# Kernel optimization log

Hardware: AMD Instinct MI355X
Metric: run time of the kernel (lower is better)

Reference implementation:

```python
import jax, jax.numpy as jnp
import numpy as np

B, T = 4096, 16384
KLEN = 50          # min(50, n_steps) with dt=1
REFRACTORY = 3.0   # self.refractory / self.dt


def setup_inputs() -> dict:
    key = jax.random.key(0)
    k1, = jax.random.split(key, 1)
    # scale so that v_reset + I_filtered/100 can cross v_th (=-55 vs reset -70)
    I_input = jax.random.normal(k1, (B, T), dtype=jnp.float32) * 2000.0
    return {
        "I_input": I_input,
        "tau_m": jnp.float32(10.0),
        "tau_s": jnp.float32(5.0),
        "v_th": jnp.float32(-55.0),
        "v_reset": jnp.float32(-70.0),
        "eta": jnp.float32(-5.0),
    }


def _srm_spikes(I_input, tau_m, tau_s, v_th, v_reset, eta):
    # synaptic kernel: (exp(-t/tau_m) - exp(-t/tau_s)) / sum
    t = jnp.arange(KLEN, dtype=jnp.float32)
    kernel = jnp.exp(-t / tau_m) - jnp.exp(-t / tau_s)
    kernel = kernel / (jnp.sum(kernel) + 1e-10)
    # 'same' convolution per trace (np.convolve semantics: kernel flipped)
    I_filt = jax.vmap(lambda x: jnp.convolve(x, kernel, mode="same"))(I_input)

    def step(ref, I_t):
        # ref: [B] refractory countdown; I_t: [B] filtered current at time t
        in_ref = ref > 0
        v_free = v_reset + I_t / 100.0
        spike = jnp.where(jnp.logical_and(~in_ref, v_free >= v_th), 1.0, 0.0)
        new_ref = jnp.where(in_ref, ref - 1.0,
                            jnp.where(spike > 0, REFRACTORY, 0.0))
        return new_ref, spike

    ref0 = jnp.zeros((I_input.shape[0],), dtype=jnp.float32)
    # original loop runs t = 1 .. n_steps-1; spikes[0] stays 0
    _, spikes_t = jax.lax.scan(step, ref0, jnp.swapaxes(I_filt[:, 1:], 0, 1))
    spikes = jnp.concatenate(
        [jnp.zeros((I_input.shape[0], 1), dtype=jnp.float32),
         jnp.swapaxes(spikes_t, 0, 1)], axis=1)
    return spikes


def reference(I_input, tau_m, tau_s, v_th, v_reset, eta):
    return _srm_spikes(I_input, tau_m, tau_s, v_th, v_reset, eta)
```

## Files before the change

### kernel.cpp

```cpp
#include <hip/hip_runtime.h>


#define TLEN   16384
#define NROWS  4096
#define KLEN   50
#define WPB    4
#define SEGS   16
#define SEGLEN 1024
#define TILEB  272

#define FGRP  256
#define FNGRP 64
#define TILEW 336

#define WS_FLAGS_OFF 256
#define WS_NEED (WS_FLAGS_OFF + (size_t)NROWS * SEGS * sizeof(int))

typedef float f4 __attribute__((ext_vector_type(4)));

__device__ __forceinline__ float uniformf(float x) {
    return __int_as_float(__builtin_amdgcn_readfirstlane(__float_as_int(x)));
}

__device__ __forceinline__ int swz(int b) { return b ^ ((b >> 4) & 7); }

__device__ __forceinline__ int map_compose(int first, int then) {
    int r = 0;
#pragma unroll
    for (int s = 0; s < 4; ++s) {
        int a = (first >> (2 * s)) & 3;
        int b = (then >> (2 * a)) & 3;
        r |= b << (2 * s);
    }
    return r;
}

__device__ float solve_thresh(float v_reset, float v_th) {
    auto tokey = [](float f) {
        unsigned u = __float_as_uint(f);
        return (u & 0x80000000u) ? ~u : (u | 0x80000000u);
    };
    auto fromkey = [](unsigned k) {
        unsigned u = (k & 0x80000000u) ? (k & 0x7FFFFFFFu) : ~k;
        return __uint_as_float(u);
    };
    const float maxf = 3.402823466e38f;
    unsigned lo = tokey(-maxf), hi = tokey(maxf);
    if (!((v_reset + maxf / 100.0f) >= v_th))
        return __uint_as_float(0x7F800000u);
    while (lo < hi) {
        unsigned mid = lo + ((hi - lo) >> 1);
        float a = fromkey(mid);
        if ((v_reset + a / 100.0f) >= v_th) hi = mid;
        else lo = mid + 1;
    }
    return fromkey(lo);
}

__global__ __launch_bounds__(64)
void setup_kernel(const float* __restrict__ p_tau_m,
                  const float* __restrict__ p_tau_s,
                  const float* __restrict__ p_v_th,
                  const float* __restrict__ p_v_reset,
                  float* __restrict__ wsf)
{
    const int lane = threadIdx.x & 63;
    const float tau_m = p_tau_m[0];
    const float tau_s = p_tau_s[0];

    float ft = (float)lane;
    float v = (lane < KLEN) ? (expf(-ft / tau_m) - expf(-ft / tau_s)) : 0.0f;

    float ksum = 0.0f;
    for (int t = 0; t < KLEN; ++t)
        ksum += __shfl(v, t, 64);
    const float kden = ksum + 1e-10f;
    const float kt = v / kden;

    if (lane < KLEN) wsf[lane] = kt;
    if (lane == 0)   wsf[KLEN] = solve_thresh(p_v_reset[0], p_v_th[0]);
}

__global__ __launch_bounds__(256)
void conv_kernel(const float* __restrict__ I,
                 const float* __restrict__ wsf,
                 float* __restrict__ out,
                 int* __restrict__ flags)
{
    __shared__ __align__(16) float tile[WPB][TILEB * 4];

    const int lane = threadIdx.x & 63;
    const int wid  = threadIdx.x >> 6;
    const int wg   = blockIdx.x * WPB + wid;
    const int row  = wg >> 4;
    const int seg  = wg & 15;

    float kt[KLEN];
#pragma unroll
    for (int t = 0; t < KLEN; ++t) kt[t] = wsf[t];
    const float athr = wsf[KLEN];

    const float* Irow = I + (size_t)row * TLEN;
    float* Orow = out + (size_t)row * TLEN;

    const int pos0 = seg * SEGLEN;
    const int t0   = pos0 + 16 * lane;

    char* tb_ = (char*)&tile[wid][0];

#pragma unroll
    for (int j = 0; j < 4; ++j) {
        f4 v = *(const f4*)(Irow + pos0 + 4 * lane + 256 * j);
        *(f4*)(tb_ + (swz(7 + lane + 64 * j) << 4)) = v;
    }
    if (lane < 7) {
        f4 h = (f4){0.0f, 0.0f, 0.0f, 0.0f};
        if (pos0 > 0) h = *(const f4*)(Irow + pos0 - 28 + 4 * lane);
        *(f4*)(tb_ + (swz(lane) << 4)) = h;
    }
    if (lane >= 57 && lane < 63) {
        f4 h = (f4){0.0f, 0.0f, 0.0f, 0.0f};
        if (pos0 + SEGLEN < TLEN)
            h = *(const f4*)(Irow + pos0 + SEGLEN + 4 * (lane - 57));
        *(f4*)(tb_ + (swz(lane + 206) << 4)) = h;
    }

    f4 wv[17];
#pragma unroll
    for (int i = 0; i < 17; ++i)
        wv[i] = *(const f4*)(tb_ + (swz(4 * lane + i) << 4));
#define WIN(m) (wv[(m) >> 2][(m) & 3])

    float acc[16];
#pragma unroll
    for (int k = 0; k < 16; ++k) acc[k] = 0.0f;
#pragma unroll
    for (int o = -25; o <= 39; ++o) {
        const float wx = WIN(o + 28);
#pragma unroll
        for (int k = 0; k < 16; ++k) {
            const int jj = k + 24 - o;
            if (jj >= 0 && jj < KLEN)
                acc[k] = fmaf(kt[jj], wx, acc[k]);
        }
    }
#undef WIN

    int m16 = 0;
#pragma unroll
    for (int k = 0; k < 16; ++k)
        m16 |= (acc[k] >= athr) ? (1 << k) : 0;
    if (t0 == 0) m16 &= ~1;
    const int rowflag = m16;

    const int sh = 4 * (lane & 3);
#pragma unroll
    for (int j = 0; j < 4; ++j) {
        const int bits = __shfl(m16, (lane >> 2) + 16 * j, 64);
        f4 o0;
        o0.x = ((bits >> (sh + 0)) & 1) ? 1.0f : 0.0f;
        o0.y = ((bits >> (sh + 1)) & 1) ? 1.0f : 0.0f;
        o0.z = ((bits >> (sh + 2)) & 1) ? 1.0f : 0.0f;
        o0.w = ((bits >> (sh + 3)) & 1) ? 1.0f : 0.0f;
        *(f4*)(Orow + pos0 + 4 * lane + 256 * j) = o0;
    }

    const unsigned long long anyb = __ballot(rowflag != 0);
    if (lane == 0) flags[wg] = (anyb != 0ULL) ? 1 : 0;
}

__global__ __launch_bounds__(256)
void fixup_kernel(const int* __restrict__ flags,
                  float* __restrict__ out)
{
    const int lane = threadIdx.x & 63;
    const int wid  = threadIdx.x >> 6;
    const int row  = blockIdx.x * WPB + wid;

    const int* pf = flags + SEGS * row;
    int any = 0;
#pragma unroll
    for (int j = 0; j < SEGS; ++j) any |= pf[j];
    if (any == 0) return;

    float* Orow = out + (size_t)row * TLEN;
    int r0 = 0;

    for (int g = 0; g < FNGRP; ++g) {
        f4 o = *(const f4*)(Orow + g * FGRP + 4 * lane);
        int cand[4];
        cand[0] = (o.x != 0.0f);
        cand[1] = (o.y != 0.0f);
        cand[2] = (o.z != 0.0f);
        cand[3] = (o.w != 0.0f);

        const int cm = cand[0] | cand[1] | cand[2] | cand[3];
        const unsigned long long anyc = __ballot(cm != 0);
        if (anyc == 0ULL) { r0 = 0; continue; }

        int s0 = 0, s1 = 1, s2 = 2, s3 = 3;
#pragma unroll
        for (int k = 0; k < 4; ++k) {
            const int c3 = cand[k] ? 3 : 0;
            s0 = (s0 > 0) ? (s0 - 1) : c3;
            s1 = (s1 > 0) ? (s1 - 1) : c3;
            s2 = (s2 > 0) ? (s2 - 1) : c3;
            s3 = (s3 > 0) ? (s3 - 1) : c3;
        }
        int P = s0 | (s1 << 2) | (s2 << 4) | (s3 << 6);

#pragma unroll
        for (int d = 1; d < 64; d <<= 1) {
            const int prev = __shfl_up(P, d, 64);
            const int comp = map_compose(prev, P);
            P = (lane >= d) ? comp : P;
        }
        const int Pprev = __shfl_up(P, 1, 64);
        const int sin0  = (lane == 0) ? r0 : ((Pprev >> (2 * r0)) & 3);
        const int Pfull = __shfl(P, 63, 64);
        r0 = (Pfull >> (2 * r0)) & 3;

        int s = sin0;
        float sp[4];
#pragma unroll
        for (int k = 0; k < 4; ++k) {
            const int spike = (s == 0) & cand[k];
            sp[k] = spike ? 1.0f : 0.0f;
            s = (s > 0) ? (s - 1) : (cand[k] ? 3 : 0);
        }
        f4 o0; o0.x = sp[0]; o0.y = sp[1]; o0.z = sp[2]; o0.w = sp[3];
        *(f4*)(Orow + g * FGRP + 4 * lane) = o0;
    }
}

__global__ __launch_bounds__(256)
void srm_kernel(const float* __restrict__ I,
                const float* __restrict__ p_tau_m,
                const float* __restrict__ p_tau_s,
                const float* __restrict__ p_v_th,
                const float* __restrict__ p_v_reset,
                float* __restrict__ out)
{
    __shared__ __align__(16) float tile[WPB][2][TILEW];

    const int lane = threadIdx.x & 63;
    const int wid  = threadIdx.x >> 6;
    const int row  = blockIdx.x * WPB + wid;

    const float tau_m   = p_tau_m[0];
    const float tau_s   = p_tau_s[0];
    const float v_th    = p_v_th[0];
    const float v_reset = p_v_reset[0];

    float ku[KLEN];
    float ksum = 0.0f;
#pragma unroll
    for (int t = 0; t < KLEN; ++t) {
        float ft = (float)t;
        float v = expf(-ft / tau_m) - expf(-ft / tau_s);
        ksum += v;
        ku[t] = uniformf(v);
    }
    const float kden = uniformf(ksum + 1e-10f);
    float kt[KLEN];
#pragma unroll
    for (int t = 0; t < KLEN; ++t) kt[t] = uniformf(ku[t] / kden);

    const float athr = uniformf(solve_thresh(v_reset, v_th));

    const float* Irow = I + (size_t)row * TLEN;
    float* Orow = out + (size_t)row * TLEN;

    float Cv[4], Nv[4], Lv[4];
    {
        f4 a = *(const f4*)(Irow + 0 * FGRP + 4 * lane);
        Cv[0] = a.x; Cv[1] = a.y; Cv[2] = a.z; Cv[3] = a.w;
        f4 c = *(const f4*)(Irow + 1 * FGRP + 4 * lane);
        Nv[0] = c.x; Nv[1] = c.y; Nv[2] = c.z; Nv[3] = c.w;
    }

    if (lane < 8) {
        f4 z = (f4){0.0f, 0.0f, 0.0f, 0.0f};
        *(f4*)&tile[wid][0][4 * lane] = z;
    }
    {
        f4 c; c.x = Cv[0]; c.y = Cv[1]; c.z = Cv[2]; c.w = Cv[3];
        *(f4*)&tile[wid][0][32 + 4 * lane] = c;
    }

    int r0 = 0;

    for (int g = 0; g < FNGRP; ++g) {
        const int cur = g & 1;
        const int nxt = cur ^ 1;

        if (g + 2 < FNGRP) {
            f4 a = *(const f4*)(Irow + (size_t)(g + 2) * FGRP + 4 * lane);
            Lv[0] = a.x; Lv[1] = a.y; Lv[2] = a.z; Lv[3] = a.w;
        } else {
            Lv[0] = Lv[1] = Lv[2] = Lv[3] = 0.0f;
        }

        f4 nv; nv.x = Nv[0]; nv.y = Nv[1]; nv.z = Nv[2]; nv.w = Nv[3];
        if (lane < 8)
            *(f4*)&tile[wid][cur][288 + 4 * lane] = nv;
        *(f4*)&tile[wid][nxt][32 + 4 * lane] = nv;
        if (lane >= 56) {
            f4 cv; cv.x = Cv[0]; cv.y = Cv[1]; cv.z = Cv[2]; cv.w = Cv[3];
            *(f4*)&tile[wid][nxt][4 * (lane - 56)] = cv;
        }

        f4 wv[15];
#pragma unroll
        for (int i = 0; i < 15; ++i)
            wv[i] = *(const f4*)&tile[wid][cur][4 * lane + 4 + 4 * i];
#define WIN(m) (wv[(m) >> 2][(m) & 3])

        float acc[4];
        acc[0] = acc[1] = acc[2] = acc[3] = 0.0f;
#pragma unroll
        for (int o = -25; o <= 27; ++o) {
            const float w = WIN(o + 28);
#pragma unroll
            for (int k = 0; k < 4; ++k) {
                const int jj = k + 24 - o;
                if (jj >= 0 && jj < KLEN)
                    acc[k] = fmaf(kt[jj], w, acc[k]);
            }
        }
#undef WIN

        const int tb = g * FGRP + 4 * lane;
        int cand[4];
#pragma unroll
        for (int k = 0; k < 4; ++k)
            cand[k] = (acc[k] >= athr) ? 1 : 0;
        cand[0] &= (tb != 0);

        const int cm = cand[0] | cand[1] | cand[2] | cand[3];
        const unsigned long long anyc = __ballot(cm != 0);

        f4 o0;
        if (anyc == 0ULL) {
            o0 = (f4){0.0f, 0.0f, 0.0f, 0.0f};
            r0 = 0;
        } else {
            int s0 = 0, s1 = 1, s2 = 2, s3 = 3;
#pragma unroll
            for (int k = 0; k < 4; ++k) {
                const int c3 = cand[k] ? 3 : 0;
                s0 = (s0 > 0) ? (s0 - 1) : c3;
                s1 = (s1 > 0) ? (s1 - 1) : c3;
                s2 = (s2 > 0) ? (s2 - 1) : c3;
                s3 = (s3 > 0) ? (s3 - 1) : c3;
            }
            int P = s0 | (s1 << 2) | (s2 << 4) | (s3 << 6);
#pragma unroll
            for (int d = 1; d < 64; d <<= 1) {
                const int prev = __shfl_up(P, d, 64);
                const int comp = map_compose(prev, P);
                P = (lane >= d) ? comp : P;
            }
            const int Pprev = __shfl_up(P, 1, 64);
            const int sin0  = (lane == 0) ? r0 : ((Pprev >> (2 * r0)) & 3);
            const int Pfull = __shfl(P, 63, 64);
            r0 = (Pfull >> (2 * r0)) & 3;

            int s = sin0;
            float sp[4];
#pragma unroll
            for (int k = 0; k < 4; ++k) {
                const int spike = (s == 0) & cand[k];
                sp[k] = spike ? 1.0f : 0.0f;
                s = (s > 0) ? (s - 1) : (cand[k] ? 3 : 0);
            }
            o0.x = sp[0]; o0.y = sp[1]; o0.z = sp[2]; o0.w = sp[3];
        }

        *(f4*)(Orow + tb) = o0;

#pragma unroll
        for (int j = 0; j < 4; ++j) { Cv[j] = Nv[j]; Nv[j] = Lv[j]; }
    }
}

extern "C" void kernel_launch(void* const* d_in, const int* in_sizes, int n_in,
                              void* d_out, int out_size, void* d_ws, size_t ws_size,
                              hipStream_t stream) {
    const float* I       = (const float*)d_in[0];
    const float* tau_m   = (const float*)d_in[1];
    const float* tau_s   = (const float*)d_in[2];
    const float* v_th    = (const float*)d_in[3];
    const float* v_reset = (const float*)d_in[4];
    float* out = (float*)d_out;

    if (ws_size >= WS_NEED) {
        float* wsf  = (float*)d_ws;
        int* flags  = (int*)((char*)d_ws + WS_FLAGS_OFF);
        setup_kernel<<<dim3(1), dim3(64), 0, stream>>>(
            tau_m, tau_s, v_th, v_reset, wsf);
        conv_kernel<<<dim3(NROWS * SEGS / WPB), dim3(256), 0, stream>>>(
            I, wsf, out, flags);
        fixup_kernel<<<dim3(NROWS / WPB), dim3(256), 0, stream>>>(flags, out);
    } else {
        srm_kernel<<<dim3(NROWS / WPB), dim3(256), 0, stream>>>(
            I, tau_m, tau_s, v_th, v_reset, out);
    }
}
```

Before: 150.7 us.

## Loop each wave over 8 segments with register prefetch of next segment

Each wavefront now processes eight consecutive 1024-sample segments of a row instead of one. The global loads for the next segment are issued into registers before the current segment's convolution runs, to hide memory latency. This also amortises the per-wave kernel-tap loads and cuts the flag count to two per row. In exchange the grid shrinks eightfold to 2048 blocks, which may reduce occupancy and latency hiding across waves, and register pressure rises from the prefetch buffers.

After: 214.7 us. +42.5%, slower.

```diff
diff --git a/kernel.cpp b/kernel.cpp
--- a/kernel.cpp
+++ b/kernel.cpp
@@ -5,7 +5,8 @@
 #define NROWS  4096
 #define KLEN   50
 #define WPB    4
-#define SEGS   16
+#define CHK    2
+#define SPW    8
 #define SEGLEN 1024
 #define TILEB  272
 
@@ -14,7 +15,7 @@
 #define TILEW 336
 
 #define WS_FLAGS_OFF 256
-#define WS_NEED (WS_FLAGS_OFF + (size_t)NROWS * SEGS * sizeof(int))
+#define WS_NEED (WS_FLAGS_OFF + (size_t)NROWS * CHK * sizeof(int))
 
 typedef float f4 __attribute__((ext_vector_type(4)));
 
@@ -92,8 +93,9 @@
     const int lane = threadIdx.x & 63;
     const int wid  = threadIdx.x >> 6;
     const int wg   = blockIdx.x * WPB + wid;
-    const int row  = wg >> 4;
-    const int seg  = wg & 15;
+    const int row  = wg >> 1;
+    const int half = wg & 1;
+    const int base = half * (SPW * SEGLEN);
 
     float kt[KLEN];
 #pragma unroll
@@ -103,66 +105,88 @@
     const float* Irow = I + (size_t)row * TLEN;
     float* Orow = out + (size_t)row * TLEN;
 
-    const int pos0 = seg * SEGLEN;
-    const int t0   = pos0 + 16 * lane;
-
     char* tb_ = (char*)&tile[wid][0];
 
-#pragma unroll
-    for (int j = 0; j < 4; ++j) {
-        f4 v = *(const f4*)(Irow + pos0 + 4 * lane + 256 * j);
-        *(f4*)(tb_ + (swz(7 + lane + 64 * j) << 4)) = v;
-    }
-    if (lane < 7) {
-        f4 h = (f4){0.0f, 0.0f, 0.0f, 0.0f};
-        if (pos0 > 0) h = *(const f4*)(Irow + pos0 - 28 + 4 * lane);
-        *(f4*)(tb_ + (swz(lane) << 4)) = h;
-    }
-    if (lane >= 57 && lane < 63) {
-        f4 h = (f4){0.0f, 0.0f, 0.0f, 0.0f};
-        if (pos0 + SEGLEN < TLEN)
-            h = *(const f4*)(Irow + pos0 + SEGLEN + 4 * (lane - 57));
-        *(f4*)(tb_ + (swz(lane + 206) << 4)) = h;
-    }
-
-    f4 wv[17];
-#pragma unroll
-    for (int i = 0; i < 17; ++i)
-        wv[i] = *(const f4*)(tb_ + (swz(4 * lane + i) << 4));
+    f4 pre[4], phl, phr;
+    {
+        const int p0 = base;
+#pragma unroll
+        for (int j = 0; j < 4; ++j)
+            pre[j] = *(const f4*)(Irow + p0 + 4 * lane + 256 * j);
+        phl = (f4){0.0f, 0.0f, 0.0f, 0.0f};
+        phr = (f4){0.0f, 0.0f, 0.0f, 0.0f};
+        if (lane < 7 && p0 > 0)
+            phl = *(const f4*)(Irow + p0 - 28 + 4 * lane);
+        if (lane >= 57 && lane < 63 && p0 + SEGLEN < TLEN)
+            phr = *(const f4*)(Irow + p0 + SEGLEN + 4 * (lane - 57));
+    }
+
+    int rowflag = 0;
+
+    for (int g = 0; g < SPW; ++g) {
+        const int pos0 = base + g * SEGLEN;
+        const int t0   = pos0 + 16 * lane;
+
+#pragma unroll
+        for (int j = 0; j < 4; ++j)
+            *(f4*)(tb_ + (swz(7 + lane + 64 * j) << 4)) = pre[j];
+        if (lane < 7)
+            *(f4*)(tb_ + (swz(lane) << 4)) = phl;
+        if (lane >= 57 && lane < 63)
+            *(f4*)(tb_ + (swz(lane + 206) << 4)) = phr;
+
+        if (g < SPW - 1) {
+            const int p1 = pos0 + SEGLEN;
+#pragma unroll
+            for (int j = 0; j < 4; ++j)
+                pre[j] = *(const f4*)(Irow + p1 + 4 * lane + 256 * j);
+            phl = (f4){0.0f, 0.0f, 0.0f, 0.0f};
+            phr = (f4){0.0f, 0.0f, 0.0f, 0.0f};
+            if (lane < 7)
+                phl = *(const f4*)(Irow + p1 - 28 + 4 * lane);
+            if (lane >= 57 && lane < 63 && p1 + SEGLEN < TLEN)
+                phr = *(const f4*)(Irow + p1 + SEGLEN + 4 * (lane - 57));
+        }
+
+        f4 wv[17];
+#pragma unroll
+        for (int i = 0; i < 17; ++i)
+            wv[i] = *(const f4*)(tb_ + (swz(4 * lane + i) << 4));
 #define WIN(m) (wv[(m) >> 2][(m) & 3])
 
-    float acc[16];
-#pragma unroll
-    for (int k = 0; k < 16; ++k) acc[k] = 0.0f;
-#pragma unroll
-    for (int o = -25; o <= 39; ++o) {
-        const float wx = WIN(o + 28);
-#pragma unroll
-        for (int k = 0; k < 16; ++k) {
-            const int jj = k + 24 - o;
-            if (jj >= 0 && jj < KLEN)
-                acc[k] = fmaf(kt[jj], wx, acc[k]);
-        }
-    }
+        float acc[16];
+#pragma unroll
+        for (int k = 0; k < 16; ++k) acc[k] = 0.0f;
+#pragma unroll
+        for (int o = -25; o <= 39; ++o) {
+            const float wx = WIN(o + 28);
+#pragma unroll
+            for (int k = 0; k < 16; ++k) {
+                const int jj = k + 24 - o;
+                if (jj >= 0 && jj < KLEN)
+                    acc[k] = fmaf(kt[jj], wx, acc[k]);
+            }
+        }
 #undef WIN
 
-    int m16 = 0;
-#pragma unroll
-    for (int k = 0; k < 16; ++k)
-        m16 |= (acc[k] >= athr) ? (1 << k) : 0;
-    if (t0 == 0) m16 &= ~1;
-    const int rowflag = m16;
-
-    const int sh = 4 * (lane & 3);
-#pragma unroll
-    for (int j = 0; j < 4; ++j) {
-        const int bits = __shfl(m16, (lane >> 2) + 16 * j, 64);
-        f4 o0;
-        o0.x = ((bits >> (sh + 0)) & 1) ? 1.0f : 0.0f;
-        o0.y = ((bits >> (sh + 1)) & 1) ? 1.0f : 0.0f;
-        o0.z = ((bits >> (sh + 2)) & 1) ? 1.0f : 0.0f;
-        o0.w = ((bits >> (sh + 3)) & 1) ? 1.0f : 0.0f;
-        *(f4*)(Orow + pos0 + 4 * lane + 256 * j) = o0;
+        int m16 = 0;
+#pragma unroll
+        for (int k = 0; k < 16; ++k)
+            m16 |= (acc[k] >= athr) ? (1 << k) : 0;
+        if (t0 == 0) m16 &= ~1;
+        rowflag |= m16;
+
+        const int sh = 4 * (lane & 3);
+#pragma unroll
+        for (int j = 0; j < 4; ++j) {
+            const int bits = __shfl(m16, (lane >> 2) + 16 * j, 64);
+            f4 o0;
+            o0.x = ((bits >> (sh + 0)) & 1) ? 1.0f : 0.0f;
+            o0.y = ((bits >> (sh + 1)) & 1) ? 1.0f : 0.0f;
+            o0.z = ((bits >> (sh + 2)) & 1) ? 1.0f : 0.0f;
+            o0.w = ((bits >> (sh + 3)) & 1) ? 1.0f : 0.0f;
+            *(f4*)(Orow + pos0 + 4 * lane + 256 * j) = o0;
+        }
     }
 
     const unsigned long long anyb = __ballot(rowflag != 0);
@@ -177,11 +201,7 @@
     const int wid  = threadIdx.x >> 6;
     const int row  = blockIdx.x * WPB + wid;
 
-    const int* pf = flags + SEGS * row;
-    int any = 0;
-#pragma unroll
-    for (int j = 0; j < SEGS; ++j) any |= pf[j];
-    if (any == 0) return;
+    if ((flags[2 * row] | flags[2 * row + 1]) == 0) return;
 
     float* Orow = out + (size_t)row * TLEN;
     int r0 = 0;
@@ -399,7 +419,7 @@
         int* flags  = (int*)((char*)d_ws + WS_FLAGS_OFF);
         setup_kernel<<<dim3(1), dim3(64), 0, stream>>>(
             tau_m, tau_s, v_th, v_reset, wsf);
-        conv_kernel<<<dim3(NROWS * SEGS / WPB), dim3(256), 0, stream>>>(
+        conv_kernel<<<dim3(NROWS * CHK / WPB), dim3(256), 0, stream>>>(
             I, wsf, out, flags);
         fixup_kernel<<<dim3(NROWS / WPB), dim3(256), 0, stream>>>(flags, out);
     } else {
```
